# Optimization experiments

Measured on AMD Instinct MI355X. Metric: run time of the kernel, lower is better.

The kernel has to match this reference:

```python
import jax, jax.numpy as jnp
import numpy as np

VOCAB = 1_000_000
EMBED_DIM = 128
BATCH = 16_384
NOISE_COUNT = 16


def setup_inputs() -> dict:
    key = jax.random.key(0)
    k1, k2, k3, k4, k5, k6 = jax.random.split(key, 6)
    embed = jax.random.uniform(k1, (EMBED_DIM, VOCAB), jnp.float32, -1.0, 1.0)
    bias = jax.random.uniform(k2, (VOCAB, 1), jnp.float32, -1.0, 1.0)
    u = jax.random.uniform(k3, (VOCAB,), jnp.float32, 1e-3, 1.0)
    freq = u / u.sum()  # normalized unigram^0.75 noise distribution
    targets = jax.random.randint(k4, (BATCH,), 0, VOCAB)
    contexts = jax.random.randint(k5, (BATCH,), 0, VOCAB)
    noises = jax.random.randint(k6, (BATCH * NOISE_COUNT,), 0, VOCAB)
    return {"embed": embed, "bias": bias, "freq": freq,
            "targets": targets, "contexts": contexts, "noises": noises,
            "noise_count": NOISE_COUNT}


def reference(embed, bias, freq, targets, contexts, noises, noise_count):
    # embed: (E, V); bias: (V, 1); freq: (V,)
    E = embed.shape[0]
    B = targets.shape[0]
    re = 10.0
    q = embed[:, targets]                      # (E, B) target embeddings
    r = embed[:, contexts]                     # (E, B) context embeddings
    b = bias[targets, 0][None, :]              # (1, B)
    s = ((r * q).sum(0)[None, :] + b) / E      # (1, B) scaled score
    # positive term: log(sigmoid(s - log(k * p(target))))
    pos = jax.nn.log_sigmoid(s - jnp.log(noise_count * freq[targets]))
    loss = pos.sum()
    # noise term: log(1 - sigmoid(tile(s,k) - log(k * p(noise)))) = log_sigmoid(-x)
    s_tiled = jnp.tile(s, (1, noise_count))    # (1, B*k) == torch.cat((s,)*k, dim=1)
    noise_loss = jax.nn.log_sigmoid(-(s_tiled - jnp.log(noise_count * freq[noises]))).sum()
    total_loss = -(loss + noise_loss) / B
    penalty = re * ((q * q).sum() + (r * r).sum()) / (E * B)
    return total_loss + penalty
```

## Files before the change

### kernel.cpp

```cpp
#include <hip/hip_runtime.h>
#include <math.h>


#define PAIRS 16
#define GSPLIT 16

__device__ __forceinline__ float log_sigmoid_f(float x) {
    return fminf(x, 0.0f) - log1pf(expf(-fabsf(x)));
}

__global__ __launch_bounds__(256) void nce_kernel(
    const float* __restrict__ embed,
    const float* __restrict__ bias,
    const float* __restrict__ freq,
    const int*   __restrict__ targets,
    const int*   __restrict__ contexts,
    const int*   __restrict__ noises,
    float*       __restrict__ block_partials,
    int V, int E, int B, int NC)
{
    __shared__ float sh_dot[PAIRS][GSPLIT + 1];
    __shared__ float sh_sq [PAIRS][GSPLIT + 1];
    __shared__ float sh_s  [PAIRS];
    __shared__ float sh_wred[4];

    const int p = threadIdx.x & (PAIRS - 1);
    const int g = threadIdx.x >> 4;
    const int j = blockIdx.x * PAIRS + p;
    const bool valid = (j < B);

    float contrib = 0.0f;

    float dot = 0.0f, sq = 0.0f;
    float lg0 = 0.0f;
    bool  has0 = false;
    float bval = 0.0f, lgt = 0.0f;
    if (valid) {
        const int t = targets[j];
        const int c = contexts[j];
        if (g < NC) {
            const int n = noises[j + (size_t)g * B];
            lg0 = logf((float)NC * freq[n]);
            has0 = true;
        }
        if (g == 0) {
            bval = bias[t];
            lgt  = logf((float)NC * freq[t]);
        }
        const int epc = E / GSPLIT;
        const int e0  = g * epc;
        const float* ct = embed + t;
        const float* cc = embed + c;
        #pragma unroll 8
        for (int e = e0; e < e0 + epc; ++e) {
            float qe = ct[(size_t)e * V];
            float re = cc[(size_t)e * V];
            dot = fmaf(qe, re, dot);
            sq  = fmaf(qe, qe, fmaf(re, re, sq));
        }
    }
    sh_dot[p][g] = dot;
    sh_sq [p][g] = sq;
    __syncthreads();

    if (threadIdx.x < PAIRS) {
        float d = 0.0f, s2 = 0.0f;
        #pragma unroll
        for (int gg = 0; gg < GSPLIT; ++gg) {
            d  += sh_dot[threadIdx.x][gg];
            s2 += sh_sq [threadIdx.x][gg];
        }
        float sval = 0.0f;
        if (valid) {
            sval = (d + bval) / (float)E;
            const float pos = log_sigmoid_f(sval - lgt);
            contrib += -pos / (float)B + 10.0f * s2 / ((float)E * (float)B);
        }
        sh_s[threadIdx.x] = sval;
    }
    __syncthreads();

    if (valid) {
        const float sval = sh_s[p];
        float nacc = 0.0f;
        if (has0) nacc = log_sigmoid_f(-(sval - lg0));
        for (int k = g + GSPLIT; k < NC; k += GSPLIT) {
            const int n = noises[j + (size_t)k * B];
            nacc += log_sigmoid_f(-(sval - logf((float)NC * freq[n])));
        }
        contrib += -nacc / (float)B;
    }

    #pragma unroll
    for (int off = 32; off > 0; off >>= 1)
        contrib += __shfl_xor(contrib, off, 64);
    const int wave = threadIdx.x >> 6;
    const int lane = threadIdx.x & 63;
    if (lane == 0) sh_wred[wave] = contrib;
    __syncthreads();
    if (threadIdx.x == 0)
        block_partials[blockIdx.x] =
            sh_wred[0] + sh_wred[1] + sh_wred[2] + sh_wred[3];
}

__global__ __launch_bounds__(256) void reduce_partials_kernel(
    const float* __restrict__ parts, int n, float* __restrict__ out)
{
    __shared__ double sh[256];
    double a = 0.0;
    for (int i = threadIdx.x; i < n; i += 256) a += (double)parts[i];
    sh[threadIdx.x] = a;
    __syncthreads();
    for (int s = 128; s > 0; s >>= 1) {
        if (threadIdx.x < s) sh[threadIdx.x] += sh[threadIdx.x + s];
        __syncthreads();
    }
    if (threadIdx.x == 0) out[0] = (float)sh[0];
}

extern "C" void kernel_launch(void* const* d_in, const int* in_sizes, int n_in,
                              void* d_out, int out_size, void* d_ws, size_t ws_size,
                              hipStream_t stream) {
    const float* embed    = (const float*)d_in[0];
    const float* bias     = (const float*)d_in[1];
    const float* freq     = (const float*)d_in[2];
    const int*   targets  = (const int*)d_in[3];
    const int*   contexts = (const int*)d_in[4];
    const int*   noises   = (const int*)d_in[5];

    const int V  = in_sizes[2];
    const int E  = in_sizes[0] / V;
    const int B  = in_sizes[3];
    const int NC = in_sizes[5] / B;

    float* partials = (float*)d_ws;

    const int nblocks = (B + PAIRS - 1) / PAIRS;

    nce_kernel<<<nblocks, 256, 0, stream>>>(
        embed, bias, freq, targets, contexts, noises, partials, V, E, B, NC);

    reduce_partials_kernel<<<1, 256, 0, stream>>>(
        partials, nblocks, (float*)d_out);
}
```

Before: 92.27 us.

## Bucket-sort embedding columns before gathering into a dense row-major buffer

Adds a histogram, scan and scatter pass that bucket-sorts the target and context column indices by vocabulary range. A gather kernel then copies columns in sorted order into a dense row-major workspace, so neighbouring threads hit nearby addresses in the strided embedding matrix. The compute kernel reads these rows as float4 vectors through an inverse permutation. This adds five extra launches, atomics, a single-block scan and a 16 MB intermediate write and read, in exchange for better locality on the scattered column gathers. The old path is kept as a fallback when E is not 128 or the workspace is too small.

```diff
diff --git a/kernel.cpp b/kernel.cpp
--- a/kernel.cpp
+++ b/kernel.cpp
@@ -2,79 +2,138 @@
 #include <math.h>
 
 
-#define PAIRS 16
-#define GSPLIT 16
+#define NB 2048
 
 __device__ __forceinline__ float log_sigmoid_f(float x) {
     return fminf(x, 0.0f) - log1pf(expf(-fabsf(x)));
 }
 
-__global__ __launch_bounds__(256) void nce_kernel(
+__device__ __forceinline__ int task_col(int i, const int* __restrict__ targets,
+                                        const int* __restrict__ contexts) {
+    const int pair = i >> 1;
+    return (i & 1) ? contexts[pair] : targets[pair];
+}
+
+__global__ __launch_bounds__(256) void hist_kernel(
+    const int* __restrict__ targets, const int* __restrict__ contexts,
+    int* __restrict__ counts, int T2, int sh)
+{
+    const int i = blockIdx.x * 256 + threadIdx.x;
+    if (i < T2) atomicAdd(&counts[task_col(i, targets, contexts) >> sh], 1);
+}
+
+__global__ __launch_bounds__(1024) void scan_kernel(
+    const int* __restrict__ counts, int* __restrict__ cursors, int nb)
+{
+    __shared__ int a[NB], b[NB];
+    for (int i = threadIdx.x; i < NB; i += 1024) a[i] = (i < nb) ? counts[i] : 0;
+    __syncthreads();
+    int* src = a; int* dst = b;
+    for (int off = 1; off < NB; off <<= 1) {
+        for (int i = threadIdx.x; i < NB; i += 1024)
+            dst[i] = src[i] + (i >= off ? src[i - off] : 0);
+        __syncthreads();
+        int* t = src; src = dst; dst = t;
+    }
+    for (int i = threadIdx.x; i < NB; i += 1024)
+        if (i < nb) cursors[i] = src[i] - counts[i];
+}
+
+__global__ __launch_bounds__(256) void scatter_kernel(
+    const int* __restrict__ targets, const int* __restrict__ contexts,
+    int* __restrict__ cursors, int* __restrict__ sorted,
+    int* __restrict__ invperm, int T2, int sh)
+{
+    const int i = blockIdx.x * 256 + threadIdx.x;
+    if (i < T2) {
+        const int col = task_col(i, targets, contexts);
+        const int pos = atomicAdd(&cursors[col >> sh], 1);
+        sorted[pos] = i;
+        invperm[i]  = pos;
+    }
+}
+
+__global__ __launch_bounds__(256) void gather_kernel(
     const float* __restrict__ embed,
-    const float* __restrict__ bias,
-    const float* __restrict__ freq,
-    const int*   __restrict__ targets,
-    const int*   __restrict__ contexts,
-    const int*   __restrict__ noises,
-    float*       __restrict__ block_partials,
-    int V, int E, int B, int NC)
-{
-    __shared__ float sh_dot[PAIRS][GSPLIT + 1];
-    __shared__ float sh_sq [PAIRS][GSPLIT + 1];
-    __shared__ float sh_s  [PAIRS];
+    const int* __restrict__ targets, const int* __restrict__ contexts,
+    const int* __restrict__ sorted, float* __restrict__ dense,
+    int V, int T2)
+{
+    const int p = threadIdx.x & 15;
+    const int g = threadIdx.x >> 4;
+    const int pos = blockIdx.x * 16 + p;
+    if (pos >= T2) return;
+    const int col = task_col(sorted[pos], targets, contexts);
+    const int e0 = g * 8;
+    const float* src = embed + col;
+    float v[8];
+    #pragma unroll
+    for (int k = 0; k < 8; ++k) v[k] = src[(size_t)(e0 + k) * V];
+    float4* dst = (float4*)(dense + (size_t)pos * 128 + e0);
+    dst[0] = make_float4(v[0], v[1], v[2], v[3]);
+    dst[1] = make_float4(v[4], v[5], v[6], v[7]);
+}
+
+__global__ __launch_bounds__(256) void compute_kernel(
+    const float* __restrict__ dense, const int* __restrict__ invperm,
+    const float* __restrict__ bias, const float* __restrict__ freq,
+    const int* __restrict__ targets, const int* __restrict__ noises,
+    float* __restrict__ partials, int B, int NC)
+{
+    __shared__ float sh_dot[16][17];
+    __shared__ float sh_sq [16][17];
+    __shared__ float sh_s  [16];
     __shared__ float sh_wred[4];
 
-    const int p = threadIdx.x & (PAIRS - 1);
+    const int p = threadIdx.x & 15;
     const int g = threadIdx.x >> 4;
-    const int j = blockIdx.x * PAIRS + p;
+    const int j = blockIdx.x * 16 + p;
     const bool valid = (j < B);
 
     float contrib = 0.0f;
-
     float dot = 0.0f, sq = 0.0f;
-    float lg0 = 0.0f;
-    bool  has0 = false;
+    float lg0 = 0.0f; bool has0 = false;
     float bval = 0.0f, lgt = 0.0f;
-    if (valid) {
-        const int t = targets[j];
-        const int c = contexts[j];
+
+    if (valid) {
         if (g < NC) {
             const int n = noises[j + (size_t)g * B];
             lg0 = logf((float)NC * freq[n]);
             has0 = true;
         }
         if (g == 0) {
+            const int t = targets[j];
             bval = bias[t];
             lgt  = logf((float)NC * freq[t]);
         }
-        const int epc = E / GSPLIT;
-        const int e0  = g * epc;
-        const float* ct = embed + t;
-        const float* cc = embed + c;
-        #pragma unroll 8
-        for (int e = e0; e < e0 + epc; ++e) {
-            float qe = ct[(size_t)e * V];
-            float re = cc[(size_t)e * V];
-            dot = fmaf(qe, re, dot);
-            sq  = fmaf(qe, qe, fmaf(re, re, sq));
-        }
+        const int e0 = g * 8;
+        const float4* qv = (const float4*)(dense + (size_t)invperm[2 * j]     * 128 + e0);
+        const float4* rv = (const float4*)(dense + (size_t)invperm[2 * j + 1] * 128 + e0);
+        const float4 q0 = qv[0], q1 = qv[1];
+        const float4 r0 = rv[0], r1 = rv[1];
+        dot = fmaf(q0.x, r0.x, fmaf(q0.y, r0.y, fmaf(q0.z, r0.z, fmaf(q0.w, r0.w,
+              fmaf(q1.x, r1.x, fmaf(q1.y, r1.y, fmaf(q1.z, r1.z, q1.w * r1.w)))))));
+        sq  = fmaf(q0.x, q0.x, fmaf(q0.y, q0.y, fmaf(q0.z, q0.z, fmaf(q0.w, q0.w,
+              fmaf(q1.x, q1.x, fmaf(q1.y, q1.y, fmaf(q1.z, q1.z, fmaf(q1.w, q1.w,
+              fmaf(r0.x, r0.x, fmaf(r0.y, r0.y, fmaf(r0.z, r0.z, fmaf(r0.w, r0.w,
+              fmaf(r1.x, r1.x, fmaf(r1.y, r1.y, fmaf(r1.z, r1.z, r1.w * r1.w)))))))))))))));
     }
     sh_dot[p][g] = dot;
     sh_sq [p][g] = sq;
     __syncthreads();
 
-    if (threadIdx.x < PAIRS) {
+    if (threadIdx.x < 16) {
         float d = 0.0f, s2 = 0.0f;
         #pragma unroll
-        for (int gg = 0; gg < GSPLIT; ++gg) {
+        for (int gg = 0; gg < 16; ++gg) {
             d  += sh_dot[threadIdx.x][gg];
             s2 += sh_sq [threadIdx.x][gg];
         }
         float sval = 0.0f;
         if (valid) {
-            sval = (d + bval) / (float)E;
+            sval = (d + bval) / 128.0f;
             const float pos = log_sigmoid_f(sval - lgt);
-            contrib += -pos / (float)B + 10.0f * s2 / ((float)E * (float)B);
+            contrib += -pos / (float)B + 10.0f * s2 / (128.0f * (float)B);
         }
         sh_s[threadIdx.x] = sval;
     }
@@ -84,7 +143,7 @@
         const float sval = sh_s[p];
         float nacc = 0.0f;
         if (has0) nacc = log_sigmoid_f(-(sval - lg0));
-        for (int k = g + GSPLIT; k < NC; k += GSPLIT) {
+        for (int k = g + 16; k < NC; k += 16) {
             const int n = noises[j + (size_t)k * B];
             nacc += log_sigmoid_f(-(sval - logf((float)NC * freq[n])));
         }
@@ -95,12 +154,10 @@
     for (int off = 32; off > 0; off >>= 1)
         contrib += __shfl_xor(contrib, off, 64);
     const int wave = threadIdx.x >> 6;
-    const int lane = threadIdx.x & 63;
-    if (lane == 0) sh_wred[wave] = contrib;
+    if ((threadIdx.x & 63) == 0) sh_wred[wave] = contrib;
     __syncthreads();
     if (threadIdx.x == 0)
-        block_partials[blockIdx.x] =
-            sh_wred[0] + sh_wred[1] + sh_wred[2] + sh_wred[3];
+        partials[blockIdx.x] = sh_wred[0] + sh_wred[1] + sh_wred[2] + sh_wred[3];
 }
 
 __global__ __launch_bounds__(256) void reduce_partials_kernel(
@@ -116,6 +173,68 @@
         __syncthreads();
     }
     if (threadIdx.x == 0) out[0] = (float)sh[0];
+}
+
+__global__ __launch_bounds__(256) void nce_fallback(
+    const float* __restrict__ embed, const float* __restrict__ bias,
+    const float* __restrict__ freq, const int* __restrict__ targets,
+    const int* __restrict__ contexts, const int* __restrict__ noises,
+    float* __restrict__ block_partials, int V, int E, int B, int NC)
+{
+    __shared__ float sh_dot[16][17];
+    __shared__ float sh_sq [16][17];
+    __shared__ float sh_s  [16];
+    __shared__ float sh_wred[4];
+    const int p = threadIdx.x & 15;
+    const int g = threadIdx.x >> 4;
+    const int j = blockIdx.x * 16 + p;
+    const bool valid = (j < B);
+    float contrib = 0.0f, dot = 0.0f, sq = 0.0f;
+    float lg0 = 0.0f; bool has0 = false; float bval = 0.0f, lgt = 0.0f;
+    if (valid) {
+        const int t = targets[j], c = contexts[j];
+        if (g < NC) { const int n = noises[j + (size_t)g * B];
+                      lg0 = logf((float)NC * freq[n]); has0 = true; }
+        if (g == 0) { bval = bias[t]; lgt = logf((float)NC * freq[t]); }
+        const int epc = E / 16, e0 = g * epc;
+        const float* ct = embed + t; const float* cc = embed + c;
+        #pragma unroll 8
+        for (int e = e0; e < e0 + epc; ++e) {
+            float qe = ct[(size_t)e * V], re = cc[(size_t)e * V];
+            dot = fmaf(qe, re, dot);
+            sq  = fmaf(qe, qe, fmaf(re, re, sq));
+        }
+    }
+    sh_dot[p][g] = dot; sh_sq[p][g] = sq;
+    __syncthreads();
+    if (threadIdx.x < 16) {
+        float d = 0.0f, s2 = 0.0f;
+        #pragma unroll
+        for (int gg = 0; gg < 16; ++gg) { d += sh_dot[threadIdx.x][gg]; s2 += sh_sq[threadIdx.x][gg]; }
+        float sval = 0.0f;
+        if (valid) {
+            sval = (d + bval) / (float)E;
+            contrib += -log_sigmoid_f(sval - lgt) / (float)B + 10.0f * s2 / ((float)E * (float)B);
+        }
+        sh_s[threadIdx.x] = sval;
+    }
+    __syncthreads();
+    if (valid) {
+        const float sval = sh_s[p];
+        float nacc = 0.0f;
+        if (has0) nacc = log_sigmoid_f(-(sval - lg0));
+        for (int k = g + 16; k < NC; k += 16) {
+            const int n = noises[j + (size_t)k * B];
+            nacc += log_sigmoid_f(-(sval - logf((float)NC * freq[n])));
+        }
+        contrib += -nacc / (float)B;
+    }
+    #pragma unroll
+    for (int off = 32; off > 0; off >>= 1) contrib += __shfl_xor(contrib, off, 64);
+    if ((threadIdx.x & 63) == 0) sh_wred[threadIdx.x >> 6] = contrib;
+    __syncthreads();
+    if (threadIdx.x == 0)
+        block_partials[blockIdx.x] = sh_wred[0] + sh_wred[1] + sh_wred[2] + sh_wred[3];
 }
 
 extern "C" void kernel_launch(void* const* d_in, const int* in_sizes, int n_in,
@@ -132,14 +251,38 @@
     const int E  = in_sizes[0] / V;
     const int B  = in_sizes[3];
     const int NC = in_sizes[5] / B;
-
-    float* partials = (float*)d_ws;
-
-    const int nblocks = (B + PAIRS - 1) / PAIRS;
-
-    nce_kernel<<<nblocks, 256, 0, stream>>>(
-        embed, bias, freq, targets, contexts, noises, partials, V, E, B, NC);
-
-    reduce_partials_kernel<<<1, 256, 0, stream>>>(
-        partials, nblocks, (float*)d_out);
-}
+    const int T2 = 2 * B;
+
+    char* ws = (char*)d_ws;
+    float* partials = (float*)ws;
+    int*   counts   = (int*)(ws + 16384);
+    int*   cursors  = (int*)(ws + 16384 + NB * 4);
+    int*   sorted   = (int*)(ws + 16384 + 2 * NB * 4);
+    int*   invperm  = sorted + T2;
+    size_t dense_off = 16384 + 2 * (size_t)NB * 4 + 2 * (size_t)T2 * 4;
+    dense_off = (dense_off + 255) & ~(size_t)255;
+    float* dense = (float*)(ws + dense_off);
+    const size_t needed = dense_off + (size_t)T2 * 128 * 4;
+
+    const int nblocks = (B + 15) / 16;
+
+    if (E == 128 && (B & 15) == 0 && ws_size >= needed) {
+        int sh = 0;
+        while ((((V - 1) >> sh) + 1) > NB) ++sh;
+        const int nb = ((V - 1) >> sh) + 1;
+
+        hipMemsetAsync(counts, 0, (size_t)NB * 4, stream);
+        hist_kernel<<<(T2 + 255) / 256, 256, 0, stream>>>(targets, contexts, counts, T2, sh);
+        scan_kernel<<<1, 1024, 0, stream>>>(counts, cursors, nb);
+        scatter_kernel<<<(T2 + 255) / 256, 256, 0, stream>>>(targets, contexts, cursors,
+                                                             sorted, invperm, T2, sh);
+        gather_kernel<<<(T2 + 15) / 16, 256, 0, stream>>>(embed, targets, contexts,
+                                                          sorted, dense, V, T2);
+        compute_kernel<<<nblocks, 256, 0, stream>>>(dense, invperm, bias, freq,
+                                                    targets, noises, partials, B, NC);
+    } else {
+        nce_fallback<<<nblocks, 256, 0, stream>>>(embed, bias, freq, targets, contexts,
+                                                  noises, partials, V, E, B, NC);
+    }
+    reduce_partials_kernel<<<1, 256, 0, stream>>>(partials, nblocks, (float*)d_out);
+}
```

Measured after the change: 102.7 us. 1.11x slower.
